# Optimization experiments

Measured on AMD Instinct MI355X. Metric: run time of the kernel, lower is better.

The kernel has to match this reference:

```python
import jax, jax.numpy as jnp
import numpy as np

B, T, I, H, C = 2048, 512, 1, 64, 2


def setup_inputs() -> dict:
    key = jax.random.key(0)
    ks = jax.random.split(key, 7)
    s = 1.0 / np.sqrt(H)  # torch LSTM/Linear init scale
    return {
        "x": jax.random.normal(ks[0], (B, T, I), jnp.float32),
        "W_ih": jax.random.uniform(ks[1], (4 * H, I), jnp.float32, -s, s),
        "W_hh": jax.random.uniform(ks[2], (4 * H, H), jnp.float32, -s, s),
        "b_ih": jax.random.uniform(ks[3], (4 * H,), jnp.float32, -s, s),
        "b_hh": jax.random.uniform(ks[4], (4 * H,), jnp.float32, -s, s),
        "W_fc": jax.random.uniform(ks[5], (C, H), jnp.float32, -s, s),
        "b_fc": jax.random.uniform(ks[6], (C,), jnp.float32, -s, s),
    }


def reference(x, W_ih, W_hh, b_ih, b_hh, W_fc, b_fc):
    # Single-layer LSTM (torch gate order: i, f, g, o), batch_first.
    # Precompute the input projection for all timesteps: [B, T, 4H]
    x_gates = jnp.einsum("bti,gi->btg", x, W_ih) + (b_ih + b_hh)

    h0 = jnp.zeros((x.shape[0], W_hh.shape[1]), x.dtype)
    c0 = h0

    def step(carry, xg_t):
        h, c = carry
        gates = xg_t + h @ W_hh.T  # [B, 4H]
        i, f, g, o = jnp.split(gates, 4, axis=-1)
        i = jax.nn.sigmoid(i)
        f = jax.nn.sigmoid(f)
        g = jnp.tanh(g)
        o = jax.nn.sigmoid(o)
        c = f * c + i * g
        h = o * jnp.tanh(c)
        return (h, c), None

    (h_T, _), _ = jax.lax.scan(step, (h0, c0), jnp.swapaxes(x_gates, 0, 1))
    # fc(h_n[-1])
    return h_T @ W_fc.T + b_fc
```

## Files before the change

kernel.cpp:

```cpp
#include <hip/hip_runtime.h>

#define LOG2E 1.44269504088896340736f

typedef short    short8  __attribute__((ext_vector_type(8)));
typedef float    floatx4 __attribute__((ext_vector_type(4)));
typedef unsigned uintx4  __attribute__((ext_vector_type(4)));

__device__ __forceinline__ unsigned pk_bf16(float lo, float hi) {
    unsigned r;
    asm("v_cvt_pk_bf16_f32 %0, %1, %2" : "=v"(r) : "v"(lo), "v"(hi));
    return r;
}
__device__ __forceinline__ float fast_tanh(float v) {
    return 1.0f - 2.0f * __builtin_amdgcn_rcpf(1.0f + __builtin_amdgcn_exp2f(2.0f * LOG2E * v));
}

__global__ void __launch_bounds__(512, 2)
lstm_mfma(const float* __restrict__ x,
          const float* __restrict__ W_ih,
          const float* __restrict__ W_hh,
          const float* __restrict__ b_ih,
          const float* __restrict__ b_hh,
          const float* __restrict__ W_fc,
          const float* __restrict__ b_fc,
          float* __restrict__ out)
{
    constexpr int T = 512;
    __shared__ unsigned hlds[16 * 32];
    __shared__ float    exch[256 * 9];

    const int tid  = threadIdx.x;
    const int w    = tid >> 6;
    const int lane = tid & 63;
    const int l15  = lane & 15;
    const int lq   = lane >> 4;
    const int b0   = blockIdx.x * 8;

    hlds[tid >= 512 ? 0 : tid] = 0u;
    short8 bf[2][2];
    #pragma unroll
    for (int j = 0; j < 2; ++j) {
        const int g = (2 * w + j) * 16 + l15;
        #pragma unroll
        for (int f = 0; f < 2; ++f) {
            const float* p = W_hh + g * 64 + 32 * f + 8 * lq;
            uintx4 uv;
            uv.x = pk_bf16(p[0], p[1]);
            uv.y = pk_bf16(p[2], p[3]);
            uv.z = pk_bf16(p[4], p[5]);
            uv.w = pk_bf16(p[6], p[7]);
            bf[j][f] = __builtin_bit_cast(short8, uv);
        }
    }
    float wihc[4], biasc[4];
    #pragma unroll
    for (int t4 = 0; t4 < 4; ++t4) {
        const int g = t4 * 64 + lane;
        wihc[t4]  = W_ih[g];
        biasc[t4] = b_ih[g] + b_hh[g];
    }

    const int aw0 = l15 * 32 + ((4 * lq +  0) ^ ((l15 & 7) << 2));
    const int aw1 = l15 * 32 + ((4 * lq + 16) ^ ((l15 & 7) << 2));
    const uintx4* ap0 = (const uintx4*)&hlds[aw0];
    const uintx4* ap1 = (const uintx4*)&hlds[aw1];
    float* ew0 = &exch[((2 * w + 0) * 16 + l15) * 9 + 4 * lq];
    float* ew1 = &exch[((2 * w + 1) * 16 + l15) * 9 + 4 * lq];
    const float* orp = &exch[lane * 9 + w];
    short* hs = (short*)hlds;
    const int hwi = (w * 32 + ((lane >> 1) ^ (w << 2))) * 2 + (lane & 1);

    const floatx4 zero = {0.0f, 0.0f, 0.0f, 0.0f};
    float c = 0.0f, h = 0.0f;
    const float* xrow = x + (long)(b0 + w) * T;

    __syncthreads();

    for (int tb = 0; tb < T; tb += 64) {
        const float xc = xrow[tb + lane];
        for (int tt = 0; tt < 64; ++tt) {
            short8 a0 = __builtin_bit_cast(short8, *ap0);
            short8 a1 = __builtin_bit_cast(short8, *ap1);
            floatx4 acc0 = __builtin_amdgcn_mfma_f32_16x16x32_bf16(a0, bf[0][0], zero, 0, 0, 0);
            acc0         = __builtin_amdgcn_mfma_f32_16x16x32_bf16(a1, bf[0][1], acc0, 0, 0, 0);
            floatx4 acc1 = __builtin_amdgcn_mfma_f32_16x16x32_bf16(a0, bf[1][0], zero, 0, 0, 0);
            acc1         = __builtin_amdgcn_mfma_f32_16x16x32_bf16(a1, bf[1][1], acc1, 0, 0, 0);
            if (lane < 32) {
                #pragma unroll
                for (int r = 0; r < 4; ++r) ew0[r] = acc0[r];
                #pragma unroll
                for (int r = 0; r < 4; ++r) ew1[r] = acc1[r];
            }
            __syncthreads();
            const float sx = __builtin_bit_cast(float,
                __builtin_amdgcn_readlane(__builtin_bit_cast(int, xc), tt));
            float gate[4];
            #pragma unroll
            for (int t4 = 0; t4 < 4; ++t4) {
                const float a = orp[t4 * 576] + fmaf(sx, wihc[t4], biasc[t4]);
                const float k = (t4 == 2) ? (2.0f * LOG2E) : (-LOG2E);
                const float rc = __builtin_amdgcn_rcpf(1.0f + __builtin_amdgcn_exp2f(k * a));
                gate[t4] = (t4 == 2) ? fmaf(-2.0f, rc, 1.0f) : rc;
            }
            c = fmaf(gate[1], c, gate[0] * gate[2]);
            h = gate[3] * fast_tanh(c);
            hs[hwi] = (short)(pk_bf16(h, h) & 0xffff);
            __syncthreads();
        }
    }

    float p0 = h * W_fc[lane];
    float p1 = h * W_fc[64 + lane];
    #pragma unroll
    for (int off = 32; off > 0; off >>= 1) {
        p0 += __shfl_down(p0, off);
        p1 += __shfl_down(p1, off);
    }
    if (lane == 0) {
        out[(b0 + w) * 2 + 0] = p0 + b_fc[0];
        out[(b0 + w) * 2 + 1] = p1 + b_fc[1];
    }
}

extern "C" void kernel_launch(void* const* d_in, const int* in_sizes, int n_in,
                              void* d_out, int out_size, void* d_ws, size_t ws_size,
                              hipStream_t stream) {
    const float* x    = (const float*)d_in[0];
    const float* W_ih = (const float*)d_in[1];
    const float* W_hh = (const float*)d_in[2];
    const float* b_ih = (const float*)d_in[3];
    const float* b_hh = (const float*)d_in[4];
    const float* W_fc = (const float*)d_in[5];
    const float* b_fc = (const float*)d_in[6];
    float* out = (float*)d_out;

    dim3 grid(256);
    dim3 block(512);
    hipLaunchKernelGGL(lstm_mfma, grid, block, 0, stream,
                       x, W_ih, W_hh, b_ih, b_hh, W_fc, b_fc, out);
}
```

Baseline: 285.7 us.

## Keep gate outputs in MFMA registers with double-buffered h and one barrier per step

The work is re-partitioned so each wave computes all four gates (i,f,g,o) for its own 16 hidden units, with W_hh as the A operand and h as the B operand. Gate activations and the cell update then run directly on the MFMA accumulators, which removes the LDS exchange buffer and one of the two __syncthreads per timestep. The h state is double-buffered in LDS so a single barrier per step is enough. The input projection is folded into the MFMA accumulator initialisation, and the block shrinks to 256 threads. The trade-off is that half the lanes (batch columns 8-15) do redundant work, and each thread now prefetches x from global memory every step.

```diff
diff --git a/kernel.cpp b/kernel.cpp
--- a/kernel.cpp
+++ b/kernel.cpp
@@ -11,11 +11,14 @@
     asm("v_cvt_pk_bf16_f32 %0, %1, %2" : "=v"(r) : "v"(lo), "v"(hi));
     return r;
 }
-__device__ __forceinline__ float fast_tanh(float v) {
+__device__ __forceinline__ float sigm(float v) {
+    return __builtin_amdgcn_rcpf(1.0f + __builtin_amdgcn_exp2f(-LOG2E * v));
+}
+__device__ __forceinline__ float tanhx(float v) {
     return 1.0f - 2.0f * __builtin_amdgcn_rcpf(1.0f + __builtin_amdgcn_exp2f(2.0f * LOG2E * v));
 }
 
-__global__ void __launch_bounds__(512, 2)
+__global__ void __launch_bounds__(256, 1)
 lstm_mfma(const float* __restrict__ x,
           const float* __restrict__ W_ih,
           const float* __restrict__ W_hh,
@@ -25,100 +28,120 @@
           const float* __restrict__ b_fc,
           float* __restrict__ out)
 {
-    constexpr int T = 512;
-    __shared__ unsigned hlds[16 * 32];
-    __shared__ float    exch[256 * 9];
+    __shared__ unsigned hlds[2 * 16 * 32];
+    __shared__ float    red[4][8][2];
 
     const int tid  = threadIdx.x;
-    const int w    = tid >> 6;
+    const int U    = tid >> 6;
     const int lane = tid & 63;
     const int l15  = lane & 15;
     const int lq   = lane >> 4;
     const int b0   = blockIdx.x * 8;
 
-    hlds[tid >= 512 ? 0 : tid] = 0u;
-    short8 bf[2][2];
     #pragma unroll
-    for (int j = 0; j < 2; ++j) {
-        const int g = (2 * w + j) * 16 + l15;
+    for (int i = 0; i < 4; ++i) hlds[tid + 256 * i] = 0u;
+
+    short8 wfrag[4][2];
+    #pragma unroll
+    for (int t4 = 0; t4 < 4; ++t4) {
+        const int grow = t4 * 64 + U * 16 + l15;
         #pragma unroll
         for (int f = 0; f < 2; ++f) {
-            const float* p = W_hh + g * 64 + 32 * f + 8 * lq;
+            const float* p = W_hh + grow * 64 + 32 * f + 8 * lq;
             uintx4 uv;
             uv.x = pk_bf16(p[0], p[1]);
             uv.y = pk_bf16(p[2], p[3]);
             uv.z = pk_bf16(p[4], p[5]);
             uv.w = pk_bf16(p[6], p[7]);
-            bf[j][f] = __builtin_bit_cast(short8, uv);
+            wfrag[t4][f] = __builtin_bit_cast(short8, uv);
         }
     }
-    float wihc[4], biasc[4];
+    float wih[4][4], bias[4][4];
     #pragma unroll
-    for (int t4 = 0; t4 < 4; ++t4) {
-        const int g = t4 * 64 + lane;
-        wihc[t4]  = W_ih[g];
-        biasc[t4] = b_ih[g] + b_hh[g];
-    }
+    for (int t4 = 0; t4 < 4; ++t4)
+        #pragma unroll
+        for (int r = 0; r < 4; ++r) {
+            const int g = t4 * 64 + U * 16 + 4 * lq + r;
+            wih[t4][r]  = W_ih[g];
+            bias[t4][r] = b_ih[g] + b_hh[g];
+        }
 
-    const int aw0 = l15 * 32 + ((4 * lq +  0) ^ ((l15 & 7) << 2));
-    const int aw1 = l15 * 32 + ((4 * lq + 16) ^ ((l15 & 7) << 2));
-    const uintx4* ap0 = (const uintx4*)&hlds[aw0];
-    const uintx4* ap1 = (const uintx4*)&hlds[aw1];
-    float* ew0 = &exch[((2 * w + 0) * 16 + l15) * 9 + 4 * lq];
-    float* ew1 = &exch[((2 * w + 1) * 16 + l15) * 9 + 4 * lq];
-    const float* orp = &exch[lane * 9 + w];
-    short* hs = (short*)hlds;
-    const int hwi = (w * 32 + ((lane >> 1) ^ (w << 2))) * 2 + (lane & 1);
+    const int swz = (l15 & 7) << 2;
+    const uintx4* rd00 = (const uintx4*)&hlds[      l15 * 32 + (( 0 + 4 * lq) ^ swz)];
+    const uintx4* rd01 = (const uintx4*)&hlds[      l15 * 32 + ((16 + 4 * lq) ^ swz)];
+    const uintx4* rd10 = (const uintx4*)&hlds[512 + l15 * 32 + (( 0 + 4 * lq) ^ swz)];
+    const uintx4* rd11 = (const uintx4*)&hlds[512 + l15 * 32 + ((16 + 4 * lq) ^ swz)];
+    unsigned* wr0 = &hlds[      l15 * 32 + ((8 * U + 2 * lq) ^ swz)];
+    unsigned* wr1 = &hlds[512 + l15 * 32 + ((8 * U + 2 * lq) ^ swz)];
 
-    const floatx4 zero = {0.0f, 0.0f, 0.0f, 0.0f};
-    float c = 0.0f, h = 0.0f;
-    const float* xrow = x + (long)(b0 + w) * T;
+    float c[4]  = {0.f, 0.f, 0.f, 0.f};
+    float hq[4] = {0.f, 0.f, 0.f, 0.f};
+
+    const float* xrow = x + (long)(b0 + (l15 & 7)) * 512;
+    float xv = xrow[0];
 
     __syncthreads();
 
-    for (int tb = 0; tb < T; tb += 64) {
-        const float xc = xrow[tb + lane];
-        for (int tt = 0; tt < 64; ++tt) {
-            short8 a0 = __builtin_bit_cast(short8, *ap0);
-            short8 a1 = __builtin_bit_cast(short8, *ap1);
-            floatx4 acc0 = __builtin_amdgcn_mfma_f32_16x16x32_bf16(a0, bf[0][0], zero, 0, 0, 0);
-            acc0         = __builtin_amdgcn_mfma_f32_16x16x32_bf16(a1, bf[0][1], acc0, 0, 0, 0);
-            floatx4 acc1 = __builtin_amdgcn_mfma_f32_16x16x32_bf16(a0, bf[1][0], zero, 0, 0, 0);
-            acc1         = __builtin_amdgcn_mfma_f32_16x16x32_bf16(a1, bf[1][1], acc1, 0, 0, 0);
-            if (lane < 32) {
-                #pragma unroll
-                for (int r = 0; r < 4; ++r) ew0[r] = acc0[r];
-                #pragma unroll
-                for (int r = 0; r < 4; ++r) ew1[r] = acc1[r];
-            }
-            __syncthreads();
-            const float sx = __builtin_bit_cast(float,
-                __builtin_amdgcn_readlane(__builtin_bit_cast(int, xc), tt));
-            float gate[4];
-            #pragma unroll
-            for (int t4 = 0; t4 < 4; ++t4) {
-                const float a = orp[t4 * 576] + fmaf(sx, wihc[t4], biasc[t4]);
-                const float k = (t4 == 2) ? (2.0f * LOG2E) : (-LOG2E);
-                const float rc = __builtin_amdgcn_rcpf(1.0f + __builtin_amdgcn_exp2f(k * a));
-                gate[t4] = (t4 == 2) ? fmaf(-2.0f, rc, 1.0f) : rc;
-            }
-            c = fmaf(gate[1], c, gate[0] * gate[2]);
-            h = gate[3] * fast_tanh(c);
-            hs[hwi] = (short)(pk_bf16(h, h) & 0xffff);
-            __syncthreads();
-        }
+#define STEP(RD0, RD1, WRP, T) do {                                              \
+    const int   tn  = ((T) < 511) ? (T) + 1 : 511;                               \
+    const float xnv = xrow[tn];                      \
+    floatx4 cin[4];                                                              \
+    _Pragma("unroll")                                                            \
+    for (int t4 = 0; t4 < 4; ++t4)                                               \
+        _Pragma("unroll")                                                        \
+        for (int r = 0; r < 4; ++r)                                              \
+            cin[t4][r] = fmaf(xv, wih[t4][r], bias[t4][r]);                      \
+    short8 hb0 = __builtin_bit_cast(short8, *(RD0));                             \
+    short8 hb1 = __builtin_bit_cast(short8, *(RD1));                             \
+    floatx4 acc[4];                                                              \
+    _Pragma("unroll")                                                            \
+    for (int t4 = 0; t4 < 4; ++t4) {                                             \
+        acc[t4] = __builtin_amdgcn_mfma_f32_16x16x32_bf16(wfrag[t4][0], hb0,     \
+                                                          cin[t4], 0, 0, 0);     \
+        acc[t4] = __builtin_amdgcn_mfma_f32_16x16x32_bf16(wfrag[t4][1], hb1,     \
+                                                          acc[t4], 0, 0, 0);     \
+    }                                                                            \
+    _Pragma("unroll")                                                            \
+    for (int r = 0; r < 4; ++r) {                                                \
+        const float ig = sigm(acc[0][r]);                                        \
+        const float fg = sigm(acc[1][r]);                                        \
+        const float gg = tanhx(acc[2][r]);                                       \
+        const float og = sigm(acc[3][r]);                                        \
+        c[r]  = fmaf(fg, c[r], ig * gg);                                         \
+        hq[r] = og * tanhx(c[r]);                                                \
+    }                                                                            \
+    if (l15 < 8) {                                                               \
+        uint2 pk;                                                                \
+        pk.x = pk_bf16(hq[0], hq[1]);                                            \
+        pk.y = pk_bf16(hq[2], hq[3]);                                            \
+        *(uint2*)(WRP) = pk;                                                     \
+    }                                                                            \
+    xv = xnv;                                                                    \
+    __syncthreads();                                                             \
+} while (0)
+
+    for (int t2 = 0; t2 < 512; t2 += 2) {
+        STEP(rd00, rd01, wr1, t2);
+        STEP(rd10, rd11, wr0, t2 + 1);
     }
+#undef STEP
 
-    float p0 = h * W_fc[lane];
-    float p1 = h * W_fc[64 + lane];
+    float p0 = 0.f, p1 = 0.f;
     #pragma unroll
-    for (int off = 32; off > 0; off >>= 1) {
-        p0 += __shfl_down(p0, off);
-        p1 += __shfl_down(p1, off);
+    for (int r = 0; r < 4; ++r) {
+        const int u = U * 16 + 4 * lq + r;
+        p0 = fmaf(hq[r], W_fc[u],      p0);
+        p1 = fmaf(hq[r], W_fc[64 + u], p1);
     }
-    if (lane == 0) {
-        out[(b0 + w) * 2 + 0] = p0 + b_fc[0];
-        out[(b0 + w) * 2 + 1] = p1 + b_fc[1];
+    p0 += __shfl_down(p0, 32);  p0 += __shfl_down(p0, 16);
+    p1 += __shfl_down(p1, 32);  p1 += __shfl_down(p1, 16);
+    if (lane < 8) { red[U][lane][0] = p0; red[U][lane][1] = p1; }
+    __syncthreads();
+    if (tid < 16) {
+        const int m = tid >> 1, cls = tid & 1;
+        const float s = red[0][m][cls] + red[1][m][cls] +
+                        red[2][m][cls] + red[3][m][cls] + b_fc[cls];
+        out[(b0 + m) * 2 + cls] = s;
     }
 }
 
@@ -135,7 +158,7 @@
     float* out = (float*)d_out;
 
     dim3 grid(256);
-    dim3 block(512);
+    dim3 block(256);
     hipLaunchKernelGGL(lstm_mfma, grid, block, 0, stream,
                        x, W_ih, W_hh, b_ih, b_hh, W_fc, b_fc, out);
 }
```

New measurement: 301.0 us. 5.3% more time.
